# Kernel tuning notes

Measured on AMD Instinct MI355X. Metric: run time of the kernel, lower is better.

## Reference

```python
import jax, jax.numpy as jnp
import numpy as np

B, S, DM = 2, 2048, 1024  # batch, seq_len, model_dim
H, HD = 16, 64            # num_heads, head_dim (H*HD == DM)


def setup_inputs() -> dict:
    key = jax.random.key(0)
    ks = jax.random.split(key, 8)
    scale = 0.02
    return {
        "k": jax.random.normal(ks[0], (B, S, DM), jnp.float32),
        "q": jax.random.normal(ks[1], (B, S, DM), jnp.float32),
        "v": jax.random.normal(ks[2], (B, S, DM), jnp.float32),
        "Wk": jax.random.normal(ks[3], (DM, H * HD), jnp.float32) * scale,
        "bk": jnp.zeros((H * HD,), jnp.float32),
        "Wq": jax.random.normal(ks[4], (DM, H * HD), jnp.float32) * scale,
        "bq": jnp.zeros((H * HD,), jnp.float32),
        "Wv": jax.random.normal(ks[5], (DM, H * HD), jnp.float32) * scale,
        "bv": jnp.zeros((H * HD,), jnp.float32),
        "Wo": jax.random.normal(ks[6], (H * HD, DM), jnp.float32) * scale,
        "bo": jnp.zeros((DM,), jnp.float32),
    }


def reference(k, q, v, Wk, bk, Wq, bq, Wv, bv, Wo, bo):
    # QKV projections (Dense with bias)
    kp = (k @ Wk + bk).reshape(B, S, H, HD)
    qp = (q @ Wq + bq).reshape(B, S, H, HD)
    vp = (v @ Wv + bv).reshape(B, S, H, HD)
    # Faithful to original: scores indexed [b, key_c, h, query_q],
    # softmax over the QUERY axis, NO 1/sqrt(head_dim) scaling.
    scores = jnp.einsum('bchd,bqhd->bchq', kp, qp)
    attn = jax.nn.softmax(scores, axis=-1)
    out = jnp.einsum('bchq,bqhd->bchd', attn, vp)  # [B, S(keys), H, HD]
    out = out.reshape(B, S, H * HD)
    return out @ Wo + bo
```

## Files before the change

kernel.cpp:

```cpp
#include <hip/hip_runtime.h>
#include <hip/hip_bf16.h>
#include <stdint.h>
#include <stddef.h>


typedef __attribute__((ext_vector_type(4))) float f32x4;
typedef __attribute__((ext_vector_type(16))) float f32x16;
typedef __attribute__((ext_vector_type(8))) short s16x8;
typedef __attribute__((ext_vector_type(4))) unsigned int u32x4;
typedef __attribute__((ext_vector_type(4))) unsigned short u16x4;

#define DEV static __device__ __forceinline__

DEV unsigned short f2bf(float x) {
  unsigned int u = __float_as_uint(x);
  u += 0x7FFF + ((u >> 16) & 1);
  return (unsigned short)(u >> 16);
}
DEV f32x4 mfma16(s16x8 a, s16x8 b, f32x4 c) {
  return __builtin_amdgcn_mfma_f32_16x16x32_bf16(a, b, c, 0, 0, 0);
}
DEV f32x16 mfma32(s16x8 a, s16x8 b, f32x16 c) {
  return __builtin_amdgcn_mfma_f32_32x32x16_bf16(a, b, c, 0, 0, 0);
}
DEV f32x4 fzero() { f32x4 z; z[0]=0.f; z[1]=0.f; z[2]=0.f; z[3]=0.f; return z; }
DEV f32x16 fzero16() {
  f32x16 z;
#pragma unroll
  for (int i = 0; i < 16; ++i) z[i] = 0.f;
  return z;
}
DEV float fexp2(float x) { return __builtin_amdgcn_exp2f(x); }

DEV void gload_lds16(const unsigned short* g, unsigned short* l) {
  __builtin_amdgcn_global_load_lds(
      (const __attribute__((address_space(1))) unsigned int*)g,
      (__attribute__((address_space(3))) unsigned int*)l, 16, 0, 0);
}

#define CVTPK(dst, a, b) \
  asm("v_cvt_pk_bf16_f32 %0, %1, %2" : "=v"(dst) : "v"(a), "v"(b))
#define PSWAP(x, y) \
  asm("v_permlane32_swap_b32 %0, %1" : "+v"(x), "+v"(y))

struct CvtArgs { const float* x[3]; unsigned short* y[3]; };

__global__ __launch_bounds__(256) void cvt_kernel(CvtArgs a) {
  const float* x = a.x[blockIdx.y];
  unsigned short* y = a.y[blockIdx.y];
  const int i = blockIdx.x * 256 + threadIdx.x;
  f32x4 v = ((const f32x4*)x)[i];
  u16x4 o;
#pragma unroll
  for (int j = 0; j < 4; ++j) o[j] = f2bf(v[j]);
  ((u16x4*)y)[i] = o;
}

struct WArgs { const float* W[4]; unsigned short* Wt[4]; };

__global__ __launch_bounds__(256) void wtrans_kernel(WArgs a) {
  const float* W = a.W[blockIdx.z];
  unsigned short* Wt = a.Wt[blockIdx.z];
  const int n0 = blockIdx.x * 32, k0 = blockIdx.y * 32;
  __shared__ float t[32][33];
  const int tx = threadIdx.x & 31, ty = threadIdx.x >> 5;
#pragma unroll
  for (int i = 0; i < 4; ++i)
    t[ty + i*8][tx] = W[(size_t)(k0 + ty + i*8) * 1024 + n0 + tx];
  __syncthreads();
#pragma unroll
  for (int i = 0; i < 4; ++i)
    Wt[(size_t)(n0 + ty + i*8) * 1024 + k0 + tx] = f2bf(t[tx][ty + i*8]);
}

struct GemArgs {
  const unsigned short* A[3];
  const unsigned short* Wt[3];
  const float* bias[3];
  void* C[3];
  int mode[3];
  float scale[3];
};

template<int BM>
__global__ __launch_bounds__(256) void gemm_kernel(GemArgs g) {
  constexpr int MF = BM / 32;
  const int z = blockIdx.z;
  const unsigned short* A  = g.A[z];
  const unsigned short* Wt = g.Wt[z];
  const float* bias = g.bias[z];
  const int mode = g.mode[z];
  const float scale = g.scale[z];
  const int m0 = blockIdx.y * BM, n0 = blockIdx.x * 128;
  const int tid = threadIdx.x;
  const int lane = tid & 63, w = tid >> 6;
  const int wm = w >> 1, wn = w & 1;
  const int lg = lane >> 4, lr = lane & 15, lx = lr & 7;

  __shared__ __align__(16) unsigned short As[BM * 64];
  __shared__ __align__(16) unsigned short Bs[128 * 64];

  f32x4 acc[MF][4];
#pragma unroll
  for (int i = 0; i < MF; ++i)
#pragma unroll
    for (int j = 0; j < 4; ++j) acc[i][j] = fzero();

  const int aStep = (mode == 2) ? 2048 * 64 : 64;
  const unsigned short* srcA[MF]; unsigned short* dstA[MF];
#pragma unroll
  for (int c = 0; c < MF; ++c) {
    int n = c*256 + tid, row = n >> 3, cg = (n & 7) ^ (row & 7);
    int s = m0 + row;
    size_t abase = (mode == 2)
        ? ((size_t)((s >> 11) * 16) * 2048 + (s & 2047)) * 64 + cg * 8
        : (size_t)s * 1024 + cg * 8;
    srcA[c] = A + abase;
    dstA[c] = &As[n * 8];
  }
  const unsigned short* srcB[4]; unsigned short* dstB[4];
#pragma unroll
  for (int c = 0; c < 4; ++c) {
    int n = c*256 + tid, row = n >> 3, cg = (n & 7) ^ (row & 7);
    srcB[c] = Wt + (size_t)(n0 + row) * 1024 + cg * 8;
    dstB[c] = &Bs[n * 8];
  }

  for (int it = 0; it < 16; ++it) {
    __syncthreads();
#pragma unroll
    for (int c = 0; c < MF; ++c) { gload_lds16(srcA[c], dstA[c]); srcA[c] += aStep; }
#pragma unroll
    for (int c = 0; c < 4; ++c)  { gload_lds16(srcB[c], dstB[c]); srcB[c] += 64; }
    __syncthreads();

    s16x8 af[2][MF], bf[2][4];
#pragma unroll
    for (int ks = 0; ks < 2; ++ks) {
#pragma unroll
      for (int mf = 0; mf < MF; ++mf) {
        int row = wm*(BM/2) + mf*16 + lr;
        af[ks][mf] = *(const s16x8*)&As[row*64 + ((ks*4 + lg) ^ lx) * 8];
      }
#pragma unroll
      for (int nf = 0; nf < 4; ++nf) {
        int row = wn*64 + nf*16 + lr;
        bf[ks][nf] = *(const s16x8*)&Bs[row*64 + ((ks*4 + lg) ^ lx) * 8];
      }
    }
#pragma unroll
    for (int mf = 0; mf < MF; ++mf)
#pragma unroll
      for (int nf = 0; nf < 4; ++nf) {
        acc[mf][nf] = mfma16(af[0][mf], bf[0][nf], acc[mf][nf]);
        acc[mf][nf] = mfma16(af[1][mf], bf[1][nf], acc[mf][nf]);
      }
  }

#pragma unroll
  for (int nf = 0; nf < 4; ++nf) {
    const int colg = n0 + wn*64 + nf*16 + lr;
    const float bi = bias[colg];
#pragma unroll
    for (int mf = 0; mf < MF; ++mf) {
      const int rowg0 = m0 + wm*(BM/2) + mf*16 + lg*4;
      if (mode == 0) {
        unsigned short* o = (unsigned short*)g.C[z];
#pragma unroll
        for (int r = 0; r < 4; ++r)
          o[(size_t)(rowg0 + r) * 1024 + colg] = f2bf((acc[mf][nf][r] + bi) * scale);
      } else if (mode == 1) {
        const int hh = colg >> 6, d = colg & 63;
        const int bb2 = rowg0 >> 11, s = rowg0 & 2047;
        u16x4 pk;
#pragma unroll
        for (int r = 0; r < 4; ++r) pk[r] = f2bf(acc[mf][nf][r] + bi);
        *(u16x4*)((unsigned short*)g.C[z] + ((size_t)((bb2*16 + hh)*64 + d)) * 2048 + s) = pk;
      } else {
        float* o = (float*)g.C[z];
#pragma unroll
        for (int r = 0; r < 4; ++r)
          o[(size_t)(rowg0 + r) * 1024 + colg] = acc[mf][nf][r] + bi;
      }
    }
  }
}

__global__ __launch_bounds__(256) void attn_kernel(
    const unsigned short* __restrict__ kp, const unsigned short* __restrict__ qp,
    const unsigned short* __restrict__ vpt, unsigned short* __restrict__ aout) {
  const int F = blockIdx.x;
  const int swz = (F & 7) * 64 + (F >> 3);
  const int bh = swz >> 4, cblk = swz & 15;
  const int b = bh >> 4, h = bh & 15;
  const int c0 = cblk * 128;
  const int tid = threadIdx.x, lane = tid & 63, w = tid >> 6;
  const int ln = lane & 31, hh = lane >> 5;

  __shared__ __align__(16) unsigned short qa_lds[2][2048];
  __shared__ __align__(16) unsigned short vb_lds[2][2048];

  const int srow = tid >> 3, sp = tid & 7, sl = sp ^ (srow & 7);
  const unsigned short* qsrc =
      qp + (size_t)(b*2048 + srow) * 1024 + h*64 + sl*8;
  const int sd = srow + 32*(sl >> 2), sjc = sl & 3;
  const unsigned short* vsrc =
      vpt + ((size_t)((b*16 + h)*64) + sd) * 2048 + sjc*8;

  s16x8 kb[4];
  {
    const unsigned short* krow =
        kp + (size_t)(b*2048 + c0 + w*32 + ln) * 1024 + h*64 + hh*8;
#pragma unroll
    for (int s = 0; s < 4; ++s) kb[s] = *(const s16x8*)(krow + s*16);
  }

  f32x16 acc0 = fzero16(), acc1 = fzero16();
  float l_run = 0.f;

  gload_lds16(qsrc, &qa_lds[0][tid*8]);
  gload_lds16(vsrc, &vb_lds[0][tid*8]);
  qsrc += 32*1024; vsrc += 32;
  __syncthreads();

  for (int jt = 0; jt < 64; ++jt) {
    const int cur = jt & 1;
    if (jt + 1 < 64) {
      gload_lds16(qsrc, &qa_lds[cur^1][tid*8]);
      gload_lds16(vsrc, &vb_lds[cur^1][tid*8]);
      qsrc += 32*1024; vsrc += 32;
    }

    s16x8 qa[4];
#pragma unroll
    for (int s = 0; s < 4; ++s) {
      const int p = (2*s + hh) ^ (ln & 7);
      qa[s] = *(const s16x8*)&qa_lds[cur][(ln*8 + p)*8];
    }
    f32x16 sc = fzero16();
#pragma unroll
    for (int s = 0; s < 4; ++s) sc = mfma32(qa[s], kb[s], sc);

    s16x8 vb[4];
#pragma unroll
    for (int t = 0; t < 4; ++t) {
      const int l = (t >> 1)*4 + (t & 1)*2 + hh;
      const int p = l ^ (ln & 7);
      vb[t] = *(const s16x8*)&vb_lds[cur][(ln*8 + p)*8];
    }

#pragma unroll
    for (int r = 0; r < 16; ++r) sc[r] = fexp2(sc[r]);
    {
      float t0 = (sc[0] + sc[1]) + (sc[2] + sc[3]);
      float t1 = (sc[4] + sc[5]) + (sc[6] + sc[7]);
      float t2 = (sc[8] + sc[9]) + (sc[10] + sc[11]);
      float t3 = (sc[12] + sc[13]) + (sc[14] + sc[15]);
      l_run += (t0 + t1) + (t2 + t3);
    }

    unsigned int a0, a1, b0, b1;
    u32x4 wv; s16x8 pa0, pa1;
    CVTPK(a0, sc[0], sc[1]);  CVTPK(b0, sc[4], sc[5]);  PSWAP(a0, b0);
    CVTPK(a1, sc[2], sc[3]);  CVTPK(b1, sc[6], sc[7]);  PSWAP(a1, b1);
    wv[0] = a0; wv[1] = a1; wv[2] = b0; wv[3] = b1;
    pa0 = __builtin_bit_cast(s16x8, wv);
    CVTPK(a0, sc[8], sc[9]);  CVTPK(b0, sc[12], sc[13]); PSWAP(a0, b0);
    CVTPK(a1, sc[10], sc[11]); CVTPK(b1, sc[14], sc[15]); PSWAP(a1, b1);
    wv[0] = a0; wv[1] = a1; wv[2] = b0; wv[3] = b1;
    pa1 = __builtin_bit_cast(s16x8, wv);

    acc0 = mfma32(vb[0], pa0, acc0);
    acc0 = mfma32(vb[1], pa1, acc0);
    acc1 = mfma32(vb[2], pa0, acc1);
    acc1 = mfma32(vb[3], pa1, acc1);

    __syncthreads();
  }

  l_run += __shfl_xor(l_run, 32);
  const float inv = 1.0f / l_run;
  unsigned short* obase =
      aout + ((size_t)bh * 2048 + c0 + w*32 + ln) * 64 + hh * 4;
#pragma unroll
  for (int dt = 0; dt < 2; ++dt)
#pragma unroll
    for (int rq = 0; rq < 4; ++rq) {
      u16x4 pk;
#pragma unroll
      for (int i = 0; i < 4; ++i) {
        const int reg = rq*4 + i;
        pk[i] = f2bf(((dt == 0) ? acc0[reg] : acc1[reg]) * inv);
      }
      *(u16x4*)(obase + dt*32 + rq*8) = pk;
    }
}

extern "C" void kernel_launch(void* const* d_in, const int* in_sizes, int n_in,
                              void* d_out, int out_size, void* d_ws, size_t ws_size,
                              hipStream_t stream) {
  (void)in_sizes; (void)n_in; (void)out_size; (void)ws_size;
  const float* k  = (const float*)d_in[0];
  const float* q  = (const float*)d_in[1];
  const float* v  = (const float*)d_in[2];
  const float* Wk = (const float*)d_in[3];
  const float* bk = (const float*)d_in[4];
  const float* Wq = (const float*)d_in[5];
  const float* bq = (const float*)d_in[6];
  const float* Wv = (const float*)d_in[7];
  const float* bv = (const float*)d_in[8];
  const float* Wo = (const float*)d_in[9];
  const float* bo = (const float*)d_in[10];

  char* ws = (char*)d_ws;
  const size_t MB = 1024 * 1024;
  unsigned short* Wkt = (unsigned short*)(ws + 0*MB);
  unsigned short* Wqt = (unsigned short*)(ws + 2*MB);
  unsigned short* Wvt = (unsigned short*)(ws + 4*MB);
  unsigned short* Wot = (unsigned short*)(ws + 6*MB);
  unsigned short* kp  = (unsigned short*)(ws + 8*MB);
  unsigned short* qp  = (unsigned short*)(ws + 16*MB);
  unsigned short* vpt = (unsigned short*)(ws + 24*MB);
  unsigned short* vc  = (unsigned short*)(ws + 32*MB);
  unsigned short* aoutb = (unsigned short*)(ws + 40*MB);
  unsigned short* kc = (unsigned short*)d_out;
  unsigned short* qc = (unsigned short*)((char*)d_out + 8*MB);

  CvtArgs ca;
  ca.x[0] = k; ca.x[1] = q; ca.x[2] = v;
  ca.y[0] = kc; ca.y[1] = qc; ca.y[2] = vc;
  cvt_kernel<<<dim3(4096, 3), 256, 0, stream>>>(ca);

  WArgs wa;
  wa.W[0] = Wk; wa.W[1] = Wq; wa.W[2] = Wv; wa.W[3] = Wo;
  wa.Wt[0] = Wkt; wa.Wt[1] = Wqt; wa.Wt[2] = Wvt; wa.Wt[3] = Wot;
  wtrans_kernel<<<dim3(32, 32, 4), 256, 0, stream>>>(wa);

  GemArgs gp;
  gp.A[0] = kc; gp.A[1] = qc; gp.A[2] = vc;
  gp.Wt[0] = Wkt; gp.Wt[1] = Wqt; gp.Wt[2] = Wvt;
  gp.bias[0] = bk; gp.bias[1] = bq; gp.bias[2] = bv;
  gp.C[0] = kp; gp.C[1] = qp; gp.C[2] = vpt;
  gp.mode[0] = 0; gp.mode[1] = 0; gp.mode[2] = 1;
  gp.scale[0] = 1.4426950408889634f;
  gp.scale[1] = 1.0f; gp.scale[2] = 1.0f;
  gemm_kernel<128><<<dim3(8, 32, 3), 256, 0, stream>>>(gp);

  attn_kernel<<<dim3(512), 256, 0, stream>>>(kp, qp, vpt, aoutb);

  GemArgs gf;
  gf.A[0] = aoutb; gf.A[1] = aoutb; gf.A[2] = aoutb;
  gf.Wt[0] = Wot; gf.Wt[1] = Wot; gf.Wt[2] = Wot;
  gf.bias[0] = bo; gf.bias[1] = bo; gf.bias[2] = bo;
  gf.C[0] = d_out; gf.C[1] = d_out; gf.C[2] = d_out;
  gf.mode[0] = 2; gf.mode[1] = 2; gf.mode[2] = 2;
  gf.scale[0] = 1.0f; gf.scale[1] = 1.0f; gf.scale[2] = 1.0f;
  gemm_kernel<64><<<dim3(8, 64, 1), 256, 0, stream>>>(gf);
}
```

Baseline: 147.0 us.

## Split query range across wave pairs, each wave handling two key row tiles

```diff
diff --git a/kernel.cpp b/kernel.cpp
--- a/kernel.cpp
+++ b/kernel.cpp
@@ -195,105 +195,154 @@
   const int b = bh >> 4, h = bh & 15;
   const int c0 = cblk * 128;
   const int tid = threadIdx.x, lane = tid & 63, w = tid >> 6;
+  const int cg = w & 1, jg = w >> 1;
   const int ln = lane & 31, hh = lane >> 5;
 
-  __shared__ __align__(16) unsigned short qa_lds[2][2048];
-  __shared__ __align__(16) unsigned short vb_lds[2][2048];
+  __shared__ __align__(16) unsigned short qa_lds[2][2][2048];
+  __shared__ __align__(16) unsigned short vb_lds[2][2][2048];
+  __shared__ float lbuf[2][2][64];
 
   const int srow = tid >> 3, sp = tid & 7, sl = sp ^ (srow & 7);
-  const unsigned short* qsrc =
+  const unsigned short* qsrc0 =
       qp + (size_t)(b*2048 + srow) * 1024 + h*64 + sl*8;
+  const unsigned short* qsrc1 = qsrc0 + (size_t)1024 * 1024;
   const int sd = srow + 32*(sl >> 2), sjc = sl & 3;
-  const unsigned short* vsrc =
+  const unsigned short* vsrc0 =
       vpt + ((size_t)((b*16 + h)*64) + sd) * 2048 + sjc*8;
-
-  s16x8 kb[4];
+  const unsigned short* vsrc1 = vsrc0 + 1024;
+
+  s16x8 kbA[4], kbB[4];
   {
-    const unsigned short* krow =
-        kp + (size_t)(b*2048 + c0 + w*32 + ln) * 1024 + h*64 + hh*8;
-#pragma unroll
-    for (int s = 0; s < 4; ++s) kb[s] = *(const s16x8*)(krow + s*16);
-  }
-
-  f32x16 acc0 = fzero16(), acc1 = fzero16();
-  float l_run = 0.f;
-
-  gload_lds16(qsrc, &qa_lds[0][tid*8]);
-  gload_lds16(vsrc, &vb_lds[0][tid*8]);
-  qsrc += 32*1024; vsrc += 32;
+    const unsigned short* krowA =
+        kp + (size_t)(b*2048 + c0 + cg*64 + ln) * 1024 + h*64 + hh*8;
+    const unsigned short* krowB = krowA + 32 * 1024;
+#pragma unroll
+    for (int s = 0; s < 4; ++s) {
+      kbA[s] = *(const s16x8*)(krowA + s*16);
+      kbB[s] = *(const s16x8*)(krowB + s*16);
+    }
+  }
+
+  f32x16 accA0 = fzero16(), accA1 = fzero16();
+  f32x16 accB0 = fzero16(), accB1 = fzero16();
+  float lA = 0.f, lB = 0.f;
+
+  gload_lds16(qsrc0, &qa_lds[0][0][tid*8]);
+  gload_lds16(qsrc1, &qa_lds[0][1][tid*8]);
+  gload_lds16(vsrc0, &vb_lds[0][0][tid*8]);
+  gload_lds16(vsrc1, &vb_lds[0][1][tid*8]);
+  qsrc0 += 32*1024; qsrc1 += 32*1024; vsrc0 += 32; vsrc1 += 32;
   __syncthreads();
 
-  for (int jt = 0; jt < 64; ++jt) {
+  for (int jt = 0; jt < 32; ++jt) {
     const int cur = jt & 1;
-    if (jt + 1 < 64) {
-      gload_lds16(qsrc, &qa_lds[cur^1][tid*8]);
-      gload_lds16(vsrc, &vb_lds[cur^1][tid*8]);
-      qsrc += 32*1024; vsrc += 32;
-    }
-
-    s16x8 qa[4];
-#pragma unroll
-    for (int s = 0; s < 4; ++s) {
-      const int p = (2*s + hh) ^ (ln & 7);
-      qa[s] = *(const s16x8*)&qa_lds[cur][(ln*8 + p)*8];
-    }
-    f32x16 sc = fzero16();
-#pragma unroll
-    for (int s = 0; s < 4; ++s) sc = mfma32(qa[s], kb[s], sc);
-
-    s16x8 vb[4];
-#pragma unroll
-    for (int t = 0; t < 4; ++t) {
-      const int l = (t >> 1)*4 + (t & 1)*2 + hh;
-      const int p = l ^ (ln & 7);
-      vb[t] = *(const s16x8*)&vb_lds[cur][(ln*8 + p)*8];
-    }
-
-#pragma unroll
-    for (int r = 0; r < 16; ++r) sc[r] = fexp2(sc[r]);
+    if (jt + 1 < 32) {
+      gload_lds16(qsrc0, &qa_lds[cur^1][0][tid*8]);
+      gload_lds16(qsrc1, &qa_lds[cur^1][1][tid*8]);
+      gload_lds16(vsrc0, &vb_lds[cur^1][0][tid*8]);
+      gload_lds16(vsrc1, &vb_lds[cur^1][1][tid*8]);
+      qsrc0 += 32*1024; qsrc1 += 32*1024; vsrc0 += 32; vsrc1 += 32;
+    }
+
+    s16x8 qa0, qa1, qa2, qa3;
     {
-      float t0 = (sc[0] + sc[1]) + (sc[2] + sc[3]);
-      float t1 = (sc[4] + sc[5]) + (sc[6] + sc[7]);
-      float t2 = (sc[8] + sc[9]) + (sc[10] + sc[11]);
-      float t3 = (sc[12] + sc[13]) + (sc[14] + sc[15]);
-      l_run += (t0 + t1) + (t2 + t3);
-    }
-
-    unsigned int a0, a1, b0, b1;
-    u32x4 wv; s16x8 pa0, pa1;
-    CVTPK(a0, sc[0], sc[1]);  CVTPK(b0, sc[4], sc[5]);  PSWAP(a0, b0);
-    CVTPK(a1, sc[2], sc[3]);  CVTPK(b1, sc[6], sc[7]);  PSWAP(a1, b1);
-    wv[0] = a0; wv[1] = a1; wv[2] = b0; wv[3] = b1;
-    pa0 = __builtin_bit_cast(s16x8, wv);
-    CVTPK(a0, sc[8], sc[9]);  CVTPK(b0, sc[12], sc[13]); PSWAP(a0, b0);
-    CVTPK(a1, sc[10], sc[11]); CVTPK(b1, sc[14], sc[15]); PSWAP(a1, b1);
-    wv[0] = a0; wv[1] = a1; wv[2] = b0; wv[3] = b1;
-    pa1 = __builtin_bit_cast(s16x8, wv);
-
-    acc0 = mfma32(vb[0], pa0, acc0);
-    acc0 = mfma32(vb[1], pa1, acc0);
-    acc1 = mfma32(vb[2], pa0, acc1);
-    acc1 = mfma32(vb[3], pa1, acc1);
+      const unsigned short* base = &qa_lds[cur][jg][0];
+      qa0 = *(const s16x8*)&base[(ln*8 + ((0 + hh) ^ (ln & 7)))*8];
+      qa1 = *(const s16x8*)&base[(ln*8 + ((2 + hh) ^ (ln & 7)))*8];
+      qa2 = *(const s16x8*)&base[(ln*8 + ((4 + hh) ^ (ln & 7)))*8];
+      qa3 = *(const s16x8*)&base[(ln*8 + ((6 + hh) ^ (ln & 7)))*8];
+    }
+    s16x8 vb0, vb1, vb2, vb3;
+    {
+      const unsigned short* base = &vb_lds[cur][jg][0];
+      vb0 = *(const s16x8*)&base[(ln*8 + ((0 + hh) ^ (ln & 7)))*8];
+      vb1 = *(const s16x8*)&base[(ln*8 + ((2 + hh) ^ (ln & 7)))*8];
+      vb2 = *(const s16x8*)&base[(ln*8 + ((4 + hh) ^ (ln & 7)))*8];
+      vb3 = *(const s16x8*)&base[(ln*8 + ((6 + hh) ^ (ln & 7)))*8];
+    }
+
+    f32x16 scA = fzero16(), scB = fzero16();
+    scA = mfma32(qa0, kbA[0], scA); scA = mfma32(qa1, kbA[1], scA);
+    scA = mfma32(qa2, kbA[2], scA); scA = mfma32(qa3, kbA[3], scA);
+    scB = mfma32(qa0, kbB[0], scB); scB = mfma32(qa1, kbB[1], scB);
+    scB = mfma32(qa2, kbB[2], scB); scB = mfma32(qa3, kbB[3], scB);
+
+#define SOFTMAX_PV(SC, LRUN, ACC0, ACC1)                                      \
+  {                                                                           \
+    _Pragma("unroll")                                                         \
+    for (int r = 0; r < 16; ++r) SC[r] = fexp2(SC[r]);                        \
+    {                                                                         \
+      float t0 = (SC[0] + SC[1]) + (SC[2] + SC[3]);                           \
+      float t1 = (SC[4] + SC[5]) + (SC[6] + SC[7]);                           \
+      float t2 = (SC[8] + SC[9]) + (SC[10] + SC[11]);                         \
+      float t3 = (SC[12] + SC[13]) + (SC[14] + SC[15]);                       \
+      LRUN += (t0 + t1) + (t2 + t3);                                          \
+    }                                                                         \
+    unsigned int a0, a1, b0, b1;                                              \
+    u32x4 wv; s16x8 pa0, pa1;                                                 \
+    CVTPK(a0, SC[0], SC[1]);  CVTPK(b0, SC[4], SC[5]);  PSWAP(a0, b0);        \
+    CVTPK(a1, SC[2], SC[3]);  CVTPK(b1, SC[6], SC[7]);  PSWAP(a1, b1);        \
+    wv[0] = a0; wv[1] = a1; wv[2] = b0; wv[3] = b1;                           \
+    pa0 = __builtin_bit_cast(s16x8, wv);                                      \
+    CVTPK(a0, SC[8], SC[9]);  CVTPK(b0, SC[12], SC[13]); PSWAP(a0, b0);       \
+    CVTPK(a1, SC[10], SC[11]); CVTPK(b1, SC[14], SC[15]); PSWAP(a1, b1);      \
+    wv[0] = a0; wv[1] = a1; wv[2] = b0; wv[3] = b1;                           \
+    pa1 = __builtin_bit_cast(s16x8, wv);                                      \
+    ACC0 = mfma32(vb0, pa0, ACC0);                                            \
+    ACC0 = mfma32(vb1, pa1, ACC0);                                            \
+    ACC1 = mfma32(vb2, pa0, ACC1);                                            \
+    ACC1 = mfma32(vb3, pa1, ACC1);                                            \
+  }
+
+    SOFTMAX_PV(scA, lA, accA0, accA1);
+    SOFTMAX_PV(scB, lB, accB0, accB1);
+#undef SOFTMAX_PV
 
     __syncthreads();
   }
 
-  l_run += __shfl_xor(l_run, 32);
-  const float inv = 1.0f / l_run;
-  unsigned short* obase =
-      aout + ((size_t)bh * 2048 + c0 + w*32 + ln) * 64 + hh * 4;
-#pragma unroll
-  for (int dt = 0; dt < 2; ++dt)
-#pragma unroll
-    for (int rq = 0; rq < 4; ++rq) {
-      u16x4 pk;
-#pragma unroll
-      for (int i = 0; i < 4; ++i) {
-        const int reg = rq*4 + i;
-        pk[i] = f2bf(((dt == 0) ? acc0[reg] : acc1[reg]) * inv);
+  float* mrg = cg ? (float*)&vb_lds[0][0][0] : (float*)&qa_lds[0][0][0];
+  if (jg == 1) {
+    lbuf[cg][0][lane] = lA; lbuf[cg][1][lane] = lB;
+#pragma unroll
+    for (int r = 0; r < 16; ++r) {
+      mrg[(r)*64 + lane]      = accA0[r];
+      mrg[(16 + r)*64 + lane] = accA1[r];
+      mrg[(32 + r)*64 + lane] = accB0[r];
+      mrg[(48 + r)*64 + lane] = accB1[r];
+    }
+  }
+  __syncthreads();
+  if (jg == 0) {
+    lA += lbuf[cg][0][lane]; lB += lbuf[cg][1][lane];
+#pragma unroll
+    for (int r = 0; r < 16; ++r) {
+      accA0[r] += mrg[(r)*64 + lane];
+      accA1[r] += mrg[(16 + r)*64 + lane];
+      accB0[r] += mrg[(32 + r)*64 + lane];
+      accB1[r] += mrg[(48 + r)*64 + lane];
+    }
+    lA += __shfl_xor(lA, 32);
+    lB += __shfl_xor(lB, 32);
+    const float invA = 1.0f / lA, invB = 1.0f / lB;
+    unsigned short* obaseA =
+        aout + ((size_t)bh * 2048 + c0 + cg*64 + ln) * 64 + hh * 4;
+    unsigned short* obaseB = obaseA + 32 * 64;
+#pragma unroll
+    for (int dt = 0; dt < 2; ++dt)
+#pragma unroll
+      for (int rq = 0; rq < 4; ++rq) {
+        u16x4 pkA, pkB;
+#pragma unroll
+        for (int i = 0; i < 4; ++i) {
+          const int reg = rq*4 + i;
+          pkA[i] = f2bf(((dt == 0) ? accA0[reg] : accA1[reg]) * invA);
+          pkB[i] = f2bf(((dt == 0) ? accB0[reg] : accB1[reg]) * invB);
+        }
+        *(u16x4*)(obaseA + dt*32 + rq*8) = pkA;
+        *(u16x4*)(obaseB + dt*32 + rq*8) = pkB;
       }
-      *(u16x4*)(obase + dt*32 + rq*8) = pk;
-    }
+  }
 }
 
 extern "C" void kernel_launch(void* const* d_in, const int* in_sizes, int n_in,
```

New measurement: 136.7 us. 7.0% less time.
